# Kernel tuning notes

Measured on AMD Instinct MI355X. Metric: run time of the kernel, lower is better.

The kernel has to match this reference:

```python
import jax, jax.numpy as jnp
import numpy as np

B, N, DEG, E, Hd, IT = 512, 81, 20, 16, 96, 4


def sudoku_neighbors():
    # 20 constraint neighbors (row/col/box, excluding self) per cell of a 9x9 grid
    n = 9
    nbrs = []
    for r in range(n):
        for c in range(n):
            s = set()
            for k in range(n):
                s.add(r * n + k)
                s.add(k * n + c)
            br, bc = (r // 3) * 3, (c // 3) * 3
            for dr in range(3):
                for dc in range(3):
                    s.add((br + dr) * n + (bc + dc))
            s.discard(r * n + c)
            nbrs.append(sorted(s))
    return np.asarray(nbrs, dtype=np.int32)  # [81, 20]


def mlp3(x, w1, b1, w2, b2, w3, b3):
    # MLP([in, h, h, out]): ReLU between layers, linear output
    x = jax.nn.relu(x @ w1 + b1)
    x = jax.nn.relu(x @ w2 + b2)
    return x @ w3 + b3


def setup_inputs() -> dict:
    key = jax.random.key(0)
    ks = iter(jax.random.split(key, 64))
    W = lambda shape, s=0.05: jax.random.normal(next(ks), shape, jnp.float32) * s
    inp = {
        'grids': jax.random.randint(next(ks), (B, N), 0, 10),
        'nbr': jnp.asarray(sudoku_neighbors()),
        'iters': IT,
        'c0': jax.random.normal(next(ks), (B * N, Hd), jnp.float32),
        'embed_w': W((10, E), 1.0),
        'in_w1': W((E, Hd)), 'in_b1': jnp.zeros((Hd,)),
        'in_w2': W((Hd, Hd)), 'in_b2': jnp.zeros((Hd,)),
        'in_w3': W((Hd, Hd)), 'in_b3': jnp.zeros((Hd,)),
        'f_w1': W((2 * Hd, Hd)), 'f_b1': jnp.zeros((Hd,)),
        'f_w2': W((Hd, Hd)), 'f_b2': jnp.zeros((Hd,)),
        'f_w3': W((Hd, Hd)), 'f_b3': jnp.zeros((Hd,)),
        'g_w1': W((2 * Hd, Hd)), 'g_b1': jnp.zeros((Hd,)),
        'g_w2': W((Hd, Hd)), 'g_b2': jnp.zeros((Hd,)),
        'g_w3': W((Hd, Hd)), 'g_b3': jnp.zeros((Hd,)),
        'lstm_wih': W((Hd, 4 * Hd)), 'lstm_whh': W((Hd, 4 * Hd)),
        'lstm_bih': jnp.zeros((4 * Hd,)), 'lstm_bhh': jnp.zeros((4 * Hd,)),
        'r_w1': W((Hd, Hd)), 'r_b1': jnp.zeros((Hd,)),
        'r_w2': W((Hd, Hd)), 'r_b2': jnp.zeros((Hd,)),
        'r_w3': W((Hd, E)), 'r_b3': jnp.zeros((E,)),
    }
    return inp


def reference(grids, nbr, iters, c0, embed_w,
              in_w1, in_b1, in_w2, in_b2, in_w3, in_b3,
              f_w1, f_b1, f_w2, f_b2, f_w3, f_b3,
              g_w1, g_b1, g_w2, g_b2, g_w3, g_b3,
              lstm_wih, lstm_whh, lstm_bih, lstm_bhh,
              r_w1, r_b1, r_w2, r_b2, r_w3, r_b3):
    X = mlp3(embed_w[grids], in_w1, in_b1, in_w2, in_b2, in_w3, in_b3)  # [B,N,Hd]
    h0 = jax.lax.stop_gradient(X).reshape(B * N, Hd)  # H = X.clone().detach()
    c = c0  # [B*N, Hd]

    def step(carry, _):
        h, c = carry
        H = h.reshape(B, N, Hd)
        Hn = H[:, nbr]  # gather neighbor states [B,N,DEG,Hd]
        pair = jnp.concatenate(
            [jnp.broadcast_to(H[:, :, None, :], Hn.shape), Hn], axis=-1)  # [B,N,DEG,2Hd]
        M = mlp3(pair, f_w1, f_b1, f_w2, f_b2, f_w3, f_b3).sum(axis=2)  # [B,N,Hd]
        x_in = mlp3(jnp.concatenate([X, M], axis=-1),
                    g_w1, g_b1, g_w2, g_b2, g_w3, g_b3).reshape(B * N, Hd)
        gates = x_in @ lstm_wih + lstm_bih + h @ lstm_whh + lstm_bhh
        i, f, g, o = jnp.split(gates, 4, axis=-1)  # torch gate order i,f,g,o
        c2 = jax.nn.sigmoid(f) * c + jax.nn.sigmoid(i) * jnp.tanh(g)
        h2 = jax.nn.sigmoid(o) * jnp.tanh(c2)
        out = mlp3(h2.reshape(B, N, Hd), r_w1, r_b1, r_w2, r_b2, r_w3, r_b3)
        return (h2, c2), out

    _, outs = jax.lax.scan(step, (h0, c), None, length=iters)
    return outs  # [iters, B, N, E]
```

## Files before the change

kernel.cpp:

```cpp
#include <hip/hip_runtime.h>
#include <math.h>

#define Bsz 512
#define Nc  81
#define Rtot (Bsz*Nc)
#define DEG 20
#define Edim 16
#define HD  96
#define NITER 4

typedef __attribute__((ext_vector_type(8))) __bf16 bf16x8;
typedef __attribute__((ext_vector_type(4))) float f32x4;

__device__ __forceinline__ float sigf(float x){ return 1.0f/(1.0f+__expf(-x)); }
__device__ __forceinline__ float tanh_fast(float x){ return 2.0f/(1.0f+__expf(-2.0f*x)) - 1.0f; }

__device__ __forceinline__ unsigned short f2bf(float f){
    union{float f; unsigned u;} v; v.f=f;
    unsigned r = v.u + 0x7fff + ((v.u>>16)&1);
    return (unsigned short)(r>>16);
}
__device__ __forceinline__ float bf2f(unsigned short s){
    union{unsigned u; float f;} v; v.u=((unsigned)s)<<16; return v.f;
}
__device__ __forceinline__ bf16x8 pack8f(const float* x){
    bf16x8 r;
    #pragma unroll
    for (int j=0;j<8;j++) r[j]=(__bf16)x[j];
    return r;
}
__device__ __forceinline__ bf16x8 ldw(const __bf16* p){ return *(const bf16x8*)p; }

__device__ __forceinline__ int swz(int row, int col){
    return row*96 + ((((col>>2) ^ (row&7))<<2) | (col&3));
}
__device__ __forceinline__ void ldtr8(const float* tp, int row, int c, float* o){
    const int r96 = row*96, rho = row&7;
    const float4 a = *(const float4*)(tp + r96 + ((((c>>2)  ) ^ rho)<<2));
    const float4 b = *(const float4*)(tp + r96 + ((((c>>2)+1) ^ rho)<<2));
    o[0]=a.x;o[1]=a.y;o[2]=a.z;o[3]=a.w;o[4]=b.x;o[5]=b.y;o[6]=b.z;o[7]=b.w;
}
__device__ __forceinline__ bf16x8 packtr8(const float* tp, int row, int c){
    float t[8]; ldtr8(tp,row,c,t); return pack8f(t);
}

#define OFF_FW1T 0
#define OFF_FW2T 18432
#define OFF_FW3T 27648
#define OFF_GW1T 36864
#define OFF_GW2T 55296
#define OFF_GW3T 64512
#define OFF_WIHT 73728
#define OFF_WHHT 110592
#define OFF_RW1T 147456
#define OFF_RW2T 156672
#define OFF_RW3T 165888
#define WT_TOTAL 167424

__global__ __launch_bounds__(256) void k_prep(
    const float* __restrict__ fw1, const float* __restrict__ fw2, const float* __restrict__ fw3,
    const float* __restrict__ gw1, const float* __restrict__ gw2, const float* __restrict__ gw3,
    const float* __restrict__ wih, const float* __restrict__ whh,
    const float* __restrict__ rw1, const float* __restrict__ rw2, const float* __restrict__ rw3,
    __bf16* __restrict__ wt)
{
    int i = blockIdx.x*256 + threadIdx.x;
    if (i >= WT_TOTAL) return;
    int j = i;
    if (j < 18432){ int n=j/96, k=j-n*96;
        wt[OFF_FW1T+j] = (__bf16)(n<96 ? fw1[k*96+n] : fw1[(96+k)*96+(n-96)]); return; }
    j -= 18432;
    if (j < 9216){ int n=j/96, k=j-n*96; wt[OFF_FW2T+j]=(__bf16)fw2[k*96+n]; return; }
    j -= 9216;
    if (j < 9216){ int n=j/96, k=j-n*96; wt[OFF_FW3T+j]=(__bf16)fw3[k*96+n]; return; }
    j -= 9216;
    if (j < 18432){ int n=j/192, k=j-n*192; wt[OFF_GW1T+j]=(__bf16)gw1[k*96+n]; return; }
    j -= 18432;
    if (j < 9216){ int n=j/96, k=j-n*96; wt[OFF_GW2T+j]=(__bf16)gw2[k*96+n]; return; }
    j -= 9216;
    if (j < 9216){ int n=j/96, k=j-n*96; wt[OFF_GW3T+j]=(__bf16)gw3[k*96+n]; return; }
    j -= 9216;
    if (j < 36864){ int n=j/96, k=j-n*96; wt[OFF_WIHT+j]=(__bf16)wih[k*384+n]; return; }
    j -= 36864;
    if (j < 36864){ int n=j/96, k=j-n*96; wt[OFF_WHHT+j]=(__bf16)whh[k*384+n]; return; }
    j -= 36864;
    if (j < 9216){ int n=j/96, k=j-n*96; wt[OFF_RW1T+j]=(__bf16)rw1[k*96+n]; return; }
    j -= 9216;
    if (j < 9216){ int n=j/96, k=j-n*96; wt[OFF_RW2T+j]=(__bf16)rw2[k*96+n]; return; }
    j -= 9216;
    { int n=j/96, k=j-n*96; wt[OFF_RW3T+j]=(__bf16)rw3[k*16+n]; }
}

__global__ __launch_bounds__(192) void k_embed(
    const int* __restrict__ grids, const float* __restrict__ embw,
    const float* __restrict__ w1, const float* __restrict__ b1,
    const float* __restrict__ w2, const float* __restrict__ b2,
    const float* __restrict__ w3, const float* __restrict__ b3,
    const float* __restrict__ c0,
    __bf16* __restrict__ X, __bf16* __restrict__ H, float* __restrict__ C)
{
    __shared__ float e[2][4][Edim];
    __shared__ float a0[2][4][HD];
    __shared__ float a1[2][4][HD];
    const int tid = threadIdx.x;
    const int rg = tid / HD, c = tid - rg*HD;
    const int r0 = blockIdx.x*8 + rg*4;

    if (c < Edim) {
        #pragma unroll
        for (int rr=0;rr<4;rr++)
            e[rg][rr][c] = embw[grids[r0+rr]*Edim + c];
    }
    __syncthreads();
    float s0,s1,s2,s3;
    s0=s1=s2=s3=b1[c];
    #pragma unroll
    for (int k=0;k<Edim;k++){
        float w=w1[k*HD+c];
        s0+=e[rg][0][k]*w; s1+=e[rg][1][k]*w;
        s2+=e[rg][2][k]*w; s3+=e[rg][3][k]*w;
    }
    a0[rg][0][c]=fmaxf(s0,0.f); a0[rg][1][c]=fmaxf(s1,0.f);
    a0[rg][2][c]=fmaxf(s2,0.f); a0[rg][3][c]=fmaxf(s3,0.f);
    __syncthreads();
    s0=s1=s2=s3=b2[c];
    #pragma unroll 4
    for (int k=0;k<HD;k++){
        float w=w2[k*HD+c];
        s0+=a0[rg][0][k]*w; s1+=a0[rg][1][k]*w;
        s2+=a0[rg][2][k]*w; s3+=a0[rg][3][k]*w;
    }
    a1[rg][0][c]=fmaxf(s0,0.f); a1[rg][1][c]=fmaxf(s1,0.f);
    a1[rg][2][c]=fmaxf(s2,0.f); a1[rg][3][c]=fmaxf(s3,0.f);
    __syncthreads();
    s0=s1=s2=s3=b3[c];
    #pragma unroll 4
    for (int k=0;k<HD;k++){
        float w=w3[k*HD+c];
        s0+=a1[rg][0][k]*w; s1+=a1[rg][1][k]*w;
        s2+=a1[rg][2][k]*w; s3+=a1[rg][3][k]*w;
    }
    X[(r0+0)*HD+c]=(__bf16)s0; H[(r0+0)*HD+c]=(__bf16)s0; C[(r0+0)*HD+c]=c0[(r0+0)*HD+c];
    X[(r0+1)*HD+c]=(__bf16)s1; H[(r0+1)*HD+c]=(__bf16)s1; C[(r0+1)*HD+c]=c0[(r0+1)*HD+c];
    X[(r0+2)*HD+c]=(__bf16)s2; H[(r0+2)*HD+c]=(__bf16)s2; C[(r0+2)*HD+c]=c0[(r0+2)*HD+c];
    X[(r0+3)*HD+c]=(__bf16)s3; H[(r0+3)*HD+c]=(__bf16)s3; C[(r0+3)*HD+c]=c0[(r0+3)*HD+c];
}

__global__ __launch_bounds__(64) void k_ab(
    const __bf16* __restrict__ H, const __bf16* __restrict__ fw1t,
    __bf16* __restrict__ Ag, __bf16* __restrict__ Bmg)
{
    const int lane = threadIdx.x & 63;
    const int row16 = lane&15, kgrp = lane>>4, ko = kgrp*8;
    const int rowA = blockIdx.x*16 + row16;
    const int rowO = blockIdx.x*16 + kgrp*4;
    bf16x8 hf[3];
    #pragma unroll
    for (int kf=0;kf<3;kf++) hf[kf]=ldw(H + (size_t)rowA*HD + kf*32 + ko);
    #pragma unroll
    for (int nf=0;nf<12;nf++){
        f32x4 c={0.f,0.f,0.f,0.f};
        #pragma unroll
        for (int kf=0;kf<3;kf++)
            c=__builtin_amdgcn_mfma_f32_16x16x32_bf16(hf[kf], ldw(fw1t+(size_t)(nf*16+row16)*HD+kf*32+ko), c, 0,0,0);
        __bf16* dst = (nf<6)? Ag : Bmg;
        int col = ((nf<6)? nf : nf-6)*16 + row16;
        #pragma unroll
        for (int q=0;q<4;q++) dst[(size_t)(rowO+q)*HD+col]=(__bf16)c[q];
    }
}

__global__ __launch_bounds__(64) void k_edge(
    const __bf16* __restrict__ Ag, const __bf16* __restrict__ Bmg,
    const int* __restrict__ nbr,
    const float* __restrict__ fb1, const __bf16* __restrict__ fw2t,
    const float* __restrict__ fb2, const __bf16* __restrict__ fw3t,
    const float* __restrict__ fb3,
    __bf16* __restrict__ M)
{
    __shared__ float accs[16*96];
    const int lane = threadIdx.x & 63;
    const int row16 = lane&15, kgrp = lane>>4, ko = kgrp*8;
    const int rowA = blockIdx.x*16 + row16;
    const int iI = rowA % Nc;
    const __bf16* BmB = Bmg + (size_t)(rowA - iI)*HD;

    bf16x8 w2f[3][6];
    #pragma unroll
    for (int kf=0; kf<3; kf++)
        #pragma unroll
        for (int nf=0; nf<6; nf++)
            w2f[kf][nf] = ldw(fw2t + (size_t)(nf*16+row16)*HD + kf*32+ko);

    float a[3][8];
    #pragma unroll
    for (int kf=0;kf<3;kf++){
        bf16x8 av = ldw(Ag + (size_t)rowA*HD + kf*32 + ko);
        #pragma unroll
        for (int j=0;j<8;j++) a[kf][j] = (float)av[j] + fb1[kf*32+ko+j];
    }
    float b2c[6], b3c[6];
    #pragma unroll
    for (int nf=0;nf<6;nf++){ b2c[nf]=fb2[nf*16+row16]; b3c[nf]=20.0f*fb3[nf*16+row16]; }

    f32x4 acc[6];
    #pragma unroll
    for (int nf=0;nf<6;nf++) acc[nf]=(f32x4){0.f,0.f,0.f,0.f};

    const int* nrow = nbr + iI*DEG;
    #pragma unroll 2
    for (int d=0; d<DEG; d++){
        int j = nrow[d];
        const __bf16* Vb = BmB + (size_t)j*HD + ko;
        bf16x8 xf[3];
        #pragma unroll
        for (int kf=0;kf<3;kf++){
            bf16x8 v = ldw(Vb + kf*32);
            float t[8];
            #pragma unroll
            for (int jj=0;jj<8;jj++) t[jj]=fmaxf(a[kf][jj] + (float)v[jj], 0.f);
            xf[kf]=pack8f(t);
        }
        f32x4 c[6];
        #pragma unroll
        for (int nf=0;nf<6;nf++) c[nf]=(f32x4){0.f,0.f,0.f,0.f};
        #pragma unroll
        for (int kf=0;kf<3;kf++)
            #pragma unroll
            for (int nf=0;nf<6;nf++)
                c[nf]=__builtin_amdgcn_mfma_f32_16x16x32_bf16(xf[kf],w2f[kf][nf],c[nf],0,0,0);
        #pragma unroll
        for (int nf=0;nf<6;nf++)
            #pragma unroll
            for (int q2=0;q2<4;q2++)
                acc[nf][q2]+=fmaxf(c[nf][q2]+b2c[nf],0.f);
    }

    #pragma unroll
    for (int nf=0;nf<6;nf++)
        #pragma unroll
        for (int q2=0;q2<4;q2++)
            accs[swz(kgrp*4+q2, nf*16+row16)]=acc[nf][q2];
    __syncthreads();

    f32x4 c2[6];
    #pragma unroll
    for (int nf=0;nf<6;nf++) c2[nf]=(f32x4){0.f,0.f,0.f,0.f};
    #pragma unroll
    for (int kf=0;kf<3;kf++){
        float h[8]; ldtr8(accs, row16, kf*32+ko, h);
        bf16x8 hif, lof;
        #pragma unroll
        for (int j=0;j<8;j++){
            unsigned short hs=f2bf(h[j]);
            union{unsigned short s; __bf16 b;} u; u.s=hs;
            hif[j]=u.b; lof[j]=(__bf16)(h[j]-bf2f(hs));
        }
        #pragma unroll
        for (int nf=0;nf<6;nf++){
            bf16x8 w3f = ldw(fw3t + (size_t)(nf*16+row16)*HD + kf*32+ko);
            c2[nf]=__builtin_amdgcn_mfma_f32_16x16x32_bf16(hif,w3f,c2[nf],0,0,0);
            c2[nf]=__builtin_amdgcn_mfma_f32_16x16x32_bf16(lof,w3f,c2[nf],0,0,0);
        }
    }
    const int rowOut = blockIdx.x*16 + kgrp*4;
    #pragma unroll
    for (int nf=0;nf<6;nf++)
        #pragma unroll
        for (int q2=0;q2<4;q2++)
            M[(size_t)(rowOut+q2)*HD + nf*16+row16] = (__bf16)(c2[nf][q2]+b3c[nf]);
}

__global__ __launch_bounds__(64) void k_fused(
    const __bf16* __restrict__ Xg, const __bf16* __restrict__ Mg,
    __bf16* __restrict__ Hg, float* __restrict__ Cg,
    __bf16* __restrict__ Ag, __bf16* __restrict__ Bmg,
    const __bf16* __restrict__ wt,
    const float* __restrict__ gb1, const float* __restrict__ gb2, const float* __restrict__ gb3,
    const float* __restrict__ bih, const float* __restrict__ bhh,
    const float* __restrict__ rb1, const float* __restrict__ rb2, const float* __restrict__ rb3,
    float* __restrict__ out, int it)
{
    __shared__ float trs[2][16*96];
    const int lane = threadIdx.x & 63;
    const int row16 = lane&15, kgrp = lane>>4, ko = kgrp*8;
    const int r0 = blockIdx.x*32;
    const int rowA0 = r0+row16,   rowA1 = r0+16+row16;
    const int rowO0 = r0+kgrp*4,  rowO1 = r0+16+kgrp*4;
    float* tp0 = trs[0]; float* tp1 = trs[1];

    const __bf16* fw1t = wt + OFF_FW1T;
    const __bf16* gw1t = wt + OFF_GW1T;
    const __bf16* gw2t = wt + OFF_GW2T;
    const __bf16* gw3t = wt + OFF_GW3T;
    const __bf16* wiht = wt + OFF_WIHT;
    const __bf16* whht = wt + OFF_WHHT;
    const __bf16* rw1t = wt + OFF_RW1T;
    const __bf16* rw2t = wt + OFF_RW2T;
    const __bf16* rw3t = wt + OFF_RW3T;

    bf16x8 xa[6], xb[6];
    #pragma unroll
    for (int kf=0;kf<3;kf++){
        xa[kf]   = ldw(Xg + (size_t)rowA0*HD + kf*32+ko);
        xb[kf]   = ldw(Xg + (size_t)rowA1*HD + kf*32+ko);
        xa[3+kf] = ldw(Mg + (size_t)rowA0*HD + kf*32+ko);
        xb[3+kf] = ldw(Mg + (size_t)rowA1*HD + kf*32+ko);
    }
    #pragma unroll
    for (int nf=0;nf<6;nf++){
        f32x4 c0={0.f,0.f,0.f,0.f}, c1={0.f,0.f,0.f,0.f};
        #pragma unroll
        for (int kf=0;kf<6;kf++){
            bf16x8 wf = ldw(gw1t + (size_t)(nf*16+row16)*192 + kf*32+ko);
            c0=__builtin_amdgcn_mfma_f32_16x16x32_bf16(xa[kf],wf,c0,0,0,0);
            c1=__builtin_amdgcn_mfma_f32_16x16x32_bf16(xb[kf],wf,c1,0,0,0);
        }
        float b=gb1[nf*16+row16];
        #pragma unroll
        for (int q=0;q<4;q++){
            tp0[swz(kgrp*4+q, nf*16+row16)]=fmaxf(c0[q]+b,0.f);
            tp1[swz(kgrp*4+q, nf*16+row16)]=fmaxf(c1[q]+b,0.f);
        }
    }
    __syncthreads();
    bf16x8 ta[3], tb[3];
    #pragma unroll
    for (int kf=0;kf<3;kf++){ ta[kf]=packtr8(tp0,row16,kf*32+ko); tb[kf]=packtr8(tp1,row16,kf*32+ko); }
    __syncthreads();
    #pragma unroll
    for (int nf=0;nf<6;nf++){
        f32x4 c0={0.f,0.f,0.f,0.f}, c1={0.f,0.f,0.f,0.f};
        #pragma unroll
        for (int kf=0;kf<3;kf++){
            bf16x8 wf = ldw(gw2t + (size_t)(nf*16+row16)*HD + kf*32+ko);
            c0=__builtin_amdgcn_mfma_f32_16x16x32_bf16(ta[kf],wf,c0,0,0,0);
            c1=__builtin_amdgcn_mfma_f32_16x16x32_bf16(tb[kf],wf,c1,0,0,0);
        }
        float b=gb2[nf*16+row16];
        #pragma unroll
        for (int q=0;q<4;q++){
            tp0[swz(kgrp*4+q, nf*16+row16)]=fmaxf(c0[q]+b,0.f);
            tp1[swz(kgrp*4+q, nf*16+row16)]=fmaxf(c1[q]+b,0.f);
        }
    }
    __syncthreads();
    #pragma unroll
    for (int kf=0;kf<3;kf++){ ta[kf]=packtr8(tp0,row16,kf*32+ko); tb[kf]=packtr8(tp1,row16,kf*32+ko); }
    __syncthreads();
    #pragma unroll
    for (int nf=0;nf<6;nf++){
        f32x4 c0={0.f,0.f,0.f,0.f}, c1={0.f,0.f,0.f,0.f};
        #pragma unroll
        for (int kf=0;kf<3;kf++){
            bf16x8 wf = ldw(gw3t + (size_t)(nf*16+row16)*HD + kf*32+ko);
            c0=__builtin_amdgcn_mfma_f32_16x16x32_bf16(ta[kf],wf,c0,0,0,0);
            c1=__builtin_amdgcn_mfma_f32_16x16x32_bf16(tb[kf],wf,c1,0,0,0);
        }
        float b=gb3[nf*16+row16];
        #pragma unroll
        for (int q=0;q<4;q++){
            tp0[swz(kgrp*4+q, nf*16+row16)]=c0[q]+b;
            tp1[swz(kgrp*4+q, nf*16+row16)]=c1[q]+b;
        }
    }
    __syncthreads();
    bf16x8 xf0[3], xf1[3];
    #pragma unroll
    for (int kf=0;kf<3;kf++){ xf0[kf]=packtr8(tp0,row16,kf*32+ko); xf1[kf]=packtr8(tp1,row16,kf*32+ko); }
    __syncthreads();

    bf16x8 hfa[3], hfb[3];
    #pragma unroll
    for (int kf=0;kf<3;kf++){
        hfa[kf]=ldw(Hg + (size_t)rowA0*HD + kf*32+ko);
        hfb[kf]=ldw(Hg + (size_t)rowA1*HD + kf*32+ko);
    }
    #pragma unroll 2
    for (int nf=0;nf<6;nf++){
        const int col = nf*16+row16;
        f32x4 g0[4], g1[4];
        #pragma unroll
        for (int g=0;g<4;g++){ g0[g]=(f32x4){0.f,0.f,0.f,0.f}; g1[g]=(f32x4){0.f,0.f,0.f,0.f}; }
        #pragma unroll
        for (int g=0;g<4;g++){
            #pragma unroll
            for (int kf=0;kf<3;kf++){
                const int kk = kf*32+ko;
                bf16x8 wx = ldw(wiht + (size_t)(g*96+col)*HD + kk);
                bf16x8 wh = ldw(whht + (size_t)(g*96+col)*HD + kk);
                g0[g]=__builtin_amdgcn_mfma_f32_16x16x32_bf16(xf0[kf],wx,g0[g],0,0,0);
                g0[g]=__builtin_amdgcn_mfma_f32_16x16x32_bf16(hfa[kf],wh,g0[g],0,0,0);
                g1[g]=__builtin_amdgcn_mfma_f32_16x16x32_bf16(xf1[kf],wx,g1[g],0,0,0);
                g1[g]=__builtin_amdgcn_mfma_f32_16x16x32_bf16(hfb[kf],wh,g1[g],0,0,0);
            }
        }
        float bi=bih[    col]+bhh[    col];
        float bf=bih[ 96+col]+bhh[ 96+col];
        float bg=bih[192+col]+bhh[192+col];
        float bo=bih[288+col]+bhh[288+col];
        #pragma unroll
        for (int q=0;q<4;q++){
            {
                size_t idx=(size_t)(rowO0+q)*HD+col;
                float cold=Cg[idx];
                float iv=sigf(g0[0][q]+bi), fv=sigf(g0[1][q]+bf);
                float gv=tanh_fast(g0[2][q]+bg), ov=sigf(g0[3][q]+bo);
                float c2v=fv*cold+iv*gv;
                float h2v=ov*tanh_fast(c2v);
                Cg[idx]=c2v; Hg[idx]=(__bf16)h2v;
                tp0[swz(kgrp*4+q,col)]=h2v;
            }
            {
                size_t idx=(size_t)(rowO1+q)*HD+col;
                float cold=Cg[idx];
                float iv=sigf(g1[0][q]+bi), fv=sigf(g1[1][q]+bf);
                float gv=tanh_fast(g1[2][q]+bg), ov=sigf(g1[3][q]+bo);
                float c2v=fv*cold+iv*gv;
                float h2v=ov*tanh_fast(c2v);
                Cg[idx]=c2v; Hg[idx]=(__bf16)h2v;
                tp1[swz(kgrp*4+q,col)]=h2v;
            }
        }
    }
    __syncthreads();

    bf16x8 hf0[3], hf1[3];
    #pragma unroll
    for (int kf=0;kf<3;kf++){ hf0[kf]=packtr8(tp0,row16,kf*32+ko); hf1[kf]=packtr8(tp1,row16,kf*32+ko); }
    __syncthreads();

    if (it < NITER-1){
        #pragma unroll
        for (int nf=0;nf<12;nf++){
            f32x4 c0={0.f,0.f,0.f,0.f}, c1={0.f,0.f,0.f,0.f};
            #pragma unroll
            for (int kf=0;kf<3;kf++){
                bf16x8 wf = ldw(fw1t + (size_t)(nf*16+row16)*HD + kf*32+ko);
                c0=__builtin_amdgcn_mfma_f32_16x16x32_bf16(hf0[kf],wf,c0,0,0,0);
                c1=__builtin_amdgcn_mfma_f32_16x16x32_bf16(hf1[kf],wf,c1,0,0,0);
            }
            __bf16* dst = (nf<6)? Ag : Bmg;
            int col = ((nf<6)? nf : nf-6)*16 + row16;
            #pragma unroll
            for (int q=0;q<4;q++){
                dst[(size_t)(rowO0+q)*HD+col]=(__bf16)c0[q];
                dst[(size_t)(rowO1+q)*HD+col]=(__bf16)c1[q];
            }
        }
    }

    #pragma unroll
    for (int nf=0;nf<6;nf++){
        f32x4 c0={0.f,0.f,0.f,0.f}, c1={0.f,0.f,0.f,0.f};
        #pragma unroll
        for (int kf=0;kf<3;kf++){
            bf16x8 wf = ldw(rw1t + (size_t)(nf*16+row16)*HD + kf*32+ko);
            c0=__builtin_amdgcn_mfma_f32_16x16x32_bf16(hf0[kf],wf,c0,0,0,0);
            c1=__builtin_amdgcn_mfma_f32_16x16x32_bf16(hf1[kf],wf,c1,0,0,0);
        }
        float b=rb1[nf*16+row16];
        #pragma unroll
        for (int q=0;q<4;q++){
            tp0[swz(kgrp*4+q, nf*16+row16)]=fmaxf(c0[q]+b,0.f);
            tp1[swz(kgrp*4+q, nf*16+row16)]=fmaxf(c1[q]+b,0.f);
        }
    }
    __syncthreads();
    #pragma unroll
    for (int kf=0;kf<3;kf++){ ta[kf]=packtr8(tp0,row16,kf*32+ko); tb[kf]=packtr8(tp1,row16,kf*32+ko); }
    __syncthreads();
    #pragma unroll
    for (int nf=0;nf<6;nf++){
        f32x4 c0={0.f,0.f,0.f,0.f}, c1={0.f,0.f,0.f,0.f};
        #pragma unroll
        for (int kf=0;kf<3;kf++){
            bf16x8 wf = ldw(rw2t + (size_t)(nf*16+row16)*HD + kf*32+ko);
            c0=__builtin_amdgcn_mfma_f32_16x16x32_bf16(ta[kf],wf,c0,0,0,0);
            c1=__builtin_amdgcn_mfma_f32_16x16x32_bf16(tb[kf],wf,c1,0,0,0);
        }
        float b=rb2[nf*16+row16];
        #pragma unroll
        for (int q=0;q<4;q++){
            tp0[swz(kgrp*4+q, nf*16+row16)]=fmaxf(c0[q]+b,0.f);
            tp1[swz(kgrp*4+q, nf*16+row16)]=fmaxf(c1[q]+b,0.f);
        }
    }
    __syncthreads();
    #pragma unroll
    for (int kf=0;kf<3;kf++){ ta[kf]=packtr8(tp0,row16,kf*32+ko); tb[kf]=packtr8(tp1,row16,kf*32+ko); }
    {
        f32x4 c0={0.f,0.f,0.f,0.f}, c1={0.f,0.f,0.f,0.f};
        #pragma unroll
        for (int kf=0;kf<3;kf++){
            bf16x8 wf = ldw(rw3t + (size_t)row16*HD + kf*32+ko);
            c0=__builtin_amdgcn_mfma_f32_16x16x32_bf16(ta[kf],wf,c0,0,0,0);
            c1=__builtin_amdgcn_mfma_f32_16x16x32_bf16(tb[kf],wf,c1,0,0,0);
        }
        float b=rb3[row16];
        #pragma unroll
        for (int q=0;q<4;q++){
            out[((size_t)it*Rtot + rowO0+q)*Edim + row16]=c0[q]+b;
            out[((size_t)it*Rtot + rowO1+q)*Edim + row16]=c1[q]+b;
        }
    }
}

extern "C" void kernel_launch(void* const* d_in, const int* in_sizes, int n_in,
                              void* d_out, int out_size, void* d_ws, size_t ws_size,
                              hipStream_t stream) {
    const int*   grids  = (const int*)  d_in[0];
    const int*   nbr    = (const int*)  d_in[1];
    const float* c0     = (const float*)d_in[3];
    const float* embw   = (const float*)d_in[4];
    const float* in_w1  = (const float*)d_in[5];
    const float* in_b1  = (const float*)d_in[6];
    const float* in_w2  = (const float*)d_in[7];
    const float* in_b2  = (const float*)d_in[8];
    const float* in_w3  = (const float*)d_in[9];
    const float* in_b3  = (const float*)d_in[10];
    const float* f_w1   = (const float*)d_in[11];
    const float* f_b1   = (const float*)d_in[12];
    const float* f_w2   = (const float*)d_in[13];
    const float* f_b2   = (const float*)d_in[14];
    const float* f_w3   = (const float*)d_in[15];
    const float* f_b3   = (const float*)d_in[16];
    const float* g_b1   = (const float*)d_in[18];
    const float* g_w1   = (const float*)d_in[17];
    const float* g_w2   = (const float*)d_in[19];
    const float* g_b2   = (const float*)d_in[20];
    const float* g_w3   = (const float*)d_in[21];
    const float* g_b3   = (const float*)d_in[22];
    const float* wih    = (const float*)d_in[23];
    const float* whh    = (const float*)d_in[24];
    const float* bih    = (const float*)d_in[25];
    const float* bhh    = (const float*)d_in[26];
    const float* r_w1   = (const float*)d_in[27];
    const float* r_b1   = (const float*)d_in[28];
    const float* r_w2   = (const float*)d_in[29];
    const float* r_b2   = (const float*)d_in[30];
    const float* r_w3   = (const float*)d_in[31];
    const float* r_b3   = (const float*)d_in[32];

    __bf16* Xb = (__bf16*)d_ws;
    __bf16* Hb = Xb + (size_t)Rtot*HD;
    float*  Cw = (float*)(Hb + (size_t)Rtot*HD);
    __bf16* Aa = (__bf16*)(Cw + (size_t)Rtot*HD);
    __bf16* Bm = Aa + (size_t)Rtot*HD;
    __bf16* Mm = Bm + (size_t)Rtot*HD;
    __bf16* wt = Mm + (size_t)Rtot*HD;
    float* out = (float*)d_out;

    const __bf16* fw1t = wt + OFF_FW1T;
    const __bf16* fw2t = wt + OFF_FW2T;
    const __bf16* fw3t = wt + OFF_FW3T;

    hipLaunchKernelGGL(k_prep, dim3((WT_TOTAL+255)/256), dim3(256), 0, stream,
        f_w1, f_w2, f_w3, g_w1, g_w2, g_w3, wih, whh, r_w1, r_w2, r_w3, wt);

    hipLaunchKernelGGL(k_embed, dim3(Rtot/8), dim3(192), 0, stream,
        grids, embw, in_w1,in_b1,in_w2,in_b2,in_w3,in_b3, c0, Xb, Hb, Cw);

    hipLaunchKernelGGL(k_ab, dim3(Rtot/16), dim3(64), 0, stream,
        Hb, fw1t, Aa, Bm);

    for (int it=0; it<NITER; ++it){
        hipLaunchKernelGGL(k_edge, dim3(Rtot/16), dim3(64), 0, stream,
            Aa, Bm, nbr, f_b1, fw2t, f_b2, fw3t, f_b3, Mm);
        hipLaunchKernelGGL(k_fused, dim3(Rtot/32), dim3(64), 0, stream,
            Xb, Mm, Hb, Cw, Aa, Bm, wt,
            g_b1, g_b2, g_b3, bih, bhh, r_b1, r_b2, r_b3,
            out, it);
    }
}
```

Measured before the change: 485.6 us.

## Fuse embed MLP with first A/B projection via MFMA, prefetch edge neighbors, halve fused tile

The scalar fp32 embed MLP and the separate k_ab launch are replaced by one MFMA-based k_embed2 that computes X and the first f_w1 projections directly. The embedding is split into bf16 hi/lo parts to keep fp32-like precision in the first layer. The c0/H copies are removed by reading X and c0 directly on iteration 0. k_edge now software-prefetches the next neighbor's rows, and k_fused processes 16 rows per block instead of 32, doubling the grid at the cost of less weight reuse per block.

```diff
diff --git a/kernel.cpp b/kernel.cpp
--- a/kernel.cpp
+++ b/kernel.cpp
@@ -55,13 +55,17 @@
 #define OFF_RW1T 147456
 #define OFF_RW2T 156672
 #define OFF_RW3T 165888
-#define WT_TOTAL 167424
+#define OFF_IW1T 167424
+#define OFF_IW2T 170496
+#define OFF_IW3T 179712
+#define WT_TOTAL 188928
 
 __global__ __launch_bounds__(256) void k_prep(
     const float* __restrict__ fw1, const float* __restrict__ fw2, const float* __restrict__ fw3,
     const float* __restrict__ gw1, const float* __restrict__ gw2, const float* __restrict__ gw3,
     const float* __restrict__ wih, const float* __restrict__ whh,
     const float* __restrict__ rw1, const float* __restrict__ rw2, const float* __restrict__ rw3,
+    const float* __restrict__ iw1, const float* __restrict__ iw2, const float* __restrict__ iw3,
     __bf16* __restrict__ wt)
 {
     int i = blockIdx.x*256 + threadIdx.x;
@@ -88,81 +92,92 @@
     j -= 9216;
     if (j < 9216){ int n=j/96, k=j-n*96; wt[OFF_RW2T+j]=(__bf16)rw2[k*96+n]; return; }
     j -= 9216;
-    { int n=j/96, k=j-n*96; wt[OFF_RW3T+j]=(__bf16)rw3[k*16+n]; }
-}
-
-__global__ __launch_bounds__(192) void k_embed(
+    if (j < 1536){ int n=j/96, k=j-n*96; wt[OFF_RW3T+j]=(__bf16)rw3[k*16+n]; return; }
+    j -= 1536;
+    if (j < 3072){ int n=j>>5, k=j&31; wt[OFF_IW1T+j]=(__bf16)iw1[(k&15)*96+n]; return; }
+    j -= 3072;
+    if (j < 9216){ int n=j/96, k=j-n*96; wt[OFF_IW2T+j]=(__bf16)iw2[k*96+n]; return; }
+    j -= 9216;
+    { int n=j/96, k=j-n*96; wt[OFF_IW3T+j]=(__bf16)iw3[k*96+n]; }
+}
+
+__global__ __launch_bounds__(64) void k_embed2(
     const int* __restrict__ grids, const float* __restrict__ embw,
-    const float* __restrict__ w1, const float* __restrict__ b1,
-    const float* __restrict__ w2, const float* __restrict__ b2,
-    const float* __restrict__ w3, const float* __restrict__ b3,
-    const float* __restrict__ c0,
-    __bf16* __restrict__ X, __bf16* __restrict__ H, float* __restrict__ C)
+    const __bf16* __restrict__ wt,
+    const float* __restrict__ ib1, const float* __restrict__ ib2, const float* __restrict__ ib3,
+    __bf16* __restrict__ X, __bf16* __restrict__ Ag, __bf16* __restrict__ Bmg)
 {
-    __shared__ float e[2][4][Edim];
-    __shared__ float a0[2][4][HD];
-    __shared__ float a1[2][4][HD];
-    const int tid = threadIdx.x;
-    const int rg = tid / HD, c = tid - rg*HD;
-    const int r0 = blockIdx.x*8 + rg*4;
-
-    if (c < Edim) {
-        #pragma unroll
-        for (int rr=0;rr<4;rr++)
-            e[rg][rr][c] = embw[grids[r0+rr]*Edim + c];
-    }
-    __syncthreads();
-    float s0,s1,s2,s3;
-    s0=s1=s2=s3=b1[c];
-    #pragma unroll
-    for (int k=0;k<Edim;k++){
-        float w=w1[k*HD+c];
-        s0+=e[rg][0][k]*w; s1+=e[rg][1][k]*w;
-        s2+=e[rg][2][k]*w; s3+=e[rg][3][k]*w;
-    }
-    a0[rg][0][c]=fmaxf(s0,0.f); a0[rg][1][c]=fmaxf(s1,0.f);
-    a0[rg][2][c]=fmaxf(s2,0.f); a0[rg][3][c]=fmaxf(s3,0.f);
-    __syncthreads();
-    s0=s1=s2=s3=b2[c];
-    #pragma unroll 4
-    for (int k=0;k<HD;k++){
-        float w=w2[k*HD+c];
-        s0+=a0[rg][0][k]*w; s1+=a0[rg][1][k]*w;
-        s2+=a0[rg][2][k]*w; s3+=a0[rg][3][k]*w;
-    }
-    a1[rg][0][c]=fmaxf(s0,0.f); a1[rg][1][c]=fmaxf(s1,0.f);
-    a1[rg][2][c]=fmaxf(s2,0.f); a1[rg][3][c]=fmaxf(s3,0.f);
-    __syncthreads();
-    s0=s1=s2=s3=b3[c];
-    #pragma unroll 4
-    for (int k=0;k<HD;k++){
-        float w=w3[k*HD+c];
-        s0+=a1[rg][0][k]*w; s1+=a1[rg][1][k]*w;
-        s2+=a1[rg][2][k]*w; s3+=a1[rg][3][k]*w;
-    }
-    X[(r0+0)*HD+c]=(__bf16)s0; H[(r0+0)*HD+c]=(__bf16)s0; C[(r0+0)*HD+c]=c0[(r0+0)*HD+c];
-    X[(r0+1)*HD+c]=(__bf16)s1; H[(r0+1)*HD+c]=(__bf16)s1; C[(r0+1)*HD+c]=c0[(r0+1)*HD+c];
-    X[(r0+2)*HD+c]=(__bf16)s2; H[(r0+2)*HD+c]=(__bf16)s2; C[(r0+2)*HD+c]=c0[(r0+2)*HD+c];
-    X[(r0+3)*HD+c]=(__bf16)s3; H[(r0+3)*HD+c]=(__bf16)s3; C[(r0+3)*HD+c]=c0[(r0+3)*HD+c];
-}
-
-__global__ __launch_bounds__(64) void k_ab(
-    const __bf16* __restrict__ H, const __bf16* __restrict__ fw1t,
-    __bf16* __restrict__ Ag, __bf16* __restrict__ Bmg)
-{
+    __shared__ float tp[16*96];
     const int lane = threadIdx.x & 63;
     const int row16 = lane&15, kgrp = lane>>4, ko = kgrp*8;
     const int rowA = blockIdx.x*16 + row16;
     const int rowO = blockIdx.x*16 + kgrp*4;
+
+    const __bf16* iw1t = wt + OFF_IW1T;
+    const __bf16* iw2t = wt + OFF_IW2T;
+    const __bf16* iw3t = wt + OFF_IW3T;
+    const __bf16* fw1t = wt + OFF_FW1T;
+
+    const int g = grids[rowA];
+    const float* ew = embw + g*Edim + (kgrp&1)*8;
+    bf16x8 ef;
+    #pragma unroll
+    for (int j=0;j<8;j++){
+        float e = ew[j];
+        if (kgrp < 2) ef[j] = (__bf16)e;
+        else          ef[j] = (__bf16)(e - bf2f(f2bf(e)));
+    }
+    #pragma unroll
+    for (int nf=0;nf<6;nf++){
+        f32x4 c={0.f,0.f,0.f,0.f};
+        c=__builtin_amdgcn_mfma_f32_16x16x32_bf16(ef, ldw(iw1t+(size_t)(nf*16+row16)*32+ko), c,0,0,0);
+        float b=ib1[nf*16+row16];
+        #pragma unroll
+        for (int q=0;q<4;q++) tp[swz(kgrp*4+q, nf*16+row16)]=fmaxf(c[q]+b,0.f);
+    }
+    __syncthreads();
+    bf16x8 ta[3];
+    #pragma unroll
+    for (int kf=0;kf<3;kf++) ta[kf]=packtr8(tp,row16,kf*32+ko);
+    __syncthreads();
+    #pragma unroll
+    for (int nf=0;nf<6;nf++){
+        f32x4 c={0.f,0.f,0.f,0.f};
+        #pragma unroll
+        for (int kf=0;kf<3;kf++)
+            c=__builtin_amdgcn_mfma_f32_16x16x32_bf16(ta[kf], ldw(iw2t+(size_t)(nf*16+row16)*HD+kf*32+ko), c,0,0,0);
+        float b=ib2[nf*16+row16];
+        #pragma unroll
+        for (int q=0;q<4;q++) tp[swz(kgrp*4+q, nf*16+row16)]=fmaxf(c[q]+b,0.f);
+    }
+    __syncthreads();
+    #pragma unroll
+    for (int kf=0;kf<3;kf++) ta[kf]=packtr8(tp,row16,kf*32+ko);
+    __syncthreads();
+    #pragma unroll
+    for (int nf=0;nf<6;nf++){
+        f32x4 c={0.f,0.f,0.f,0.f};
+        #pragma unroll
+        for (int kf=0;kf<3;kf++)
+            c=__builtin_amdgcn_mfma_f32_16x16x32_bf16(ta[kf], ldw(iw3t+(size_t)(nf*16+row16)*HD+kf*32+ko), c,0,0,0);
+        float b=ib3[nf*16+row16];
+        #pragma unroll
+        for (int q=0;q<4;q++){
+            float v=c[q]+b;
+            X[(size_t)(rowO+q)*HD + nf*16+row16]=(__bf16)v;
+            tp[swz(kgrp*4+q, nf*16+row16)]=v;
+        }
+    }
+    __syncthreads();
     bf16x8 hf[3];
     #pragma unroll
-    for (int kf=0;kf<3;kf++) hf[kf]=ldw(H + (size_t)rowA*HD + kf*32 + ko);
+    for (int kf=0;kf<3;kf++) hf[kf]=packtr8(tp,row16,kf*32+ko);
     #pragma unroll
     for (int nf=0;nf<12;nf++){
         f32x4 c={0.f,0.f,0.f,0.f};
         #pragma unroll
         for (int kf=0;kf<3;kf++)
-            c=__builtin_amdgcn_mfma_f32_16x16x32_bf16(hf[kf], ldw(fw1t+(size_t)(nf*16+row16)*HD+kf*32+ko), c, 0,0,0);
+            c=__builtin_amdgcn_mfma_f32_16x16x32_bf16(hf[kf], ldw(fw1t+(size_t)(nf*16+row16)*HD+kf*32+ko), c,0,0,0);
         __bf16* dst = (nf<6)? Ag : Bmg;
         int col = ((nf<6)? nf : nf-6)*16 + row16;
         #pragma unroll
@@ -183,7 +198,7 @@
     const int row16 = lane&15, kgrp = lane>>4, ko = kgrp*8;
     const int rowA = blockIdx.x*16 + row16;
     const int iI = rowA % Nc;
-    const __bf16* BmB = Bmg + (size_t)(rowA - iI)*HD;
+    const __bf16* BmB = Bmg + (size_t)(rowA - iI)*HD + ko;
 
     bf16x8 w2f[3][6];
     #pragma unroll
@@ -208,18 +223,31 @@
     for (int nf=0;nf<6;nf++) acc[nf]=(f32x4){0.f,0.f,0.f,0.f};
 
     const int* nrow = nbr + iI*DEG;
+    bf16x8 v0,v1,v2;
+    {
+        const __bf16* Vb = BmB + (size_t)nrow[0]*HD;
+        v0=ldw(Vb); v1=ldw(Vb+32); v2=ldw(Vb+64);
+    }
     #pragma unroll 2
     for (int d=0; d<DEG; d++){
-        int j = nrow[d];
-        const __bf16* Vb = BmB + (size_t)j*HD + ko;
+        bf16x8 n0,n1,n2;
+        {
+            int dn = (d+1<DEG)? d+1 : 0;
+            const __bf16* Vb = BmB + (size_t)nrow[dn]*HD;
+            n0=ldw(Vb); n1=ldw(Vb+32); n2=ldw(Vb+64);
+        }
         bf16x8 xf[3];
-        #pragma unroll
-        for (int kf=0;kf<3;kf++){
-            bf16x8 v = ldw(Vb + kf*32);
+        {
             float t[8];
             #pragma unroll
-            for (int jj=0;jj<8;jj++) t[jj]=fmaxf(a[kf][jj] + (float)v[jj], 0.f);
-            xf[kf]=pack8f(t);
+            for (int jj=0;jj<8;jj++) t[jj]=fmaxf(a[0][jj]+(float)v0[jj],0.f);
+            xf[0]=pack8f(t);
+            #pragma unroll
+            for (int jj=0;jj<8;jj++) t[jj]=fmaxf(a[1][jj]+(float)v1[jj],0.f);
+            xf[1]=pack8f(t);
+            #pragma unroll
+            for (int jj=0;jj<8;jj++) t[jj]=fmaxf(a[2][jj]+(float)v2[jj],0.f);
+            xf[2]=pack8f(t);
         }
         f32x4 c[6];
         #pragma unroll
@@ -234,6 +262,7 @@
             #pragma unroll
             for (int q2=0;q2<4;q2++)
                 acc[nf][q2]+=fmaxf(c[nf][q2]+b2c[nf],0.f);
+        v0=n0; v1=n1; v2=n2;
     }
 
     #pragma unroll
@@ -273,21 +302,20 @@
 
 __global__ __launch_bounds__(64) void k_fused(
     const __bf16* __restrict__ Xg, const __bf16* __restrict__ Mg,
-    __bf16* __restrict__ Hg, float* __restrict__ Cg,
+    const __bf16* __restrict__ Hin, __bf16* __restrict__ Hout,
+    const float* __restrict__ Cin, float* __restrict__ Cout,
     __bf16* __restrict__ Ag, __bf16* __restrict__ Bmg,
     const __bf16* __restrict__ wt,
     const float* __restrict__ gb1, const float* __restrict__ gb2, const float* __restrict__ gb3,
     const float* __restrict__ bih, const float* __restrict__ bhh,
     const float* __restrict__ rb1, const float* __restrict__ rb2, const float* __restrict__ rb3,
-    float* __restrict__ out, int it)
+    float* __restrict__ out, int it, int wab)
 {
-    __shared__ float trs[2][16*96];
+    __shared__ float tp[16*96];
     const int lane = threadIdx.x & 63;
     const int row16 = lane&15, kgrp = lane>>4, ko = kgrp*8;
-    const int r0 = blockIdx.x*32;
-    const int rowA0 = r0+row16,   rowA1 = r0+16+row16;
-    const int rowO0 = r0+kgrp*4,  rowO1 = r0+16+kgrp*4;
-    float* tp0 = trs[0]; float* tp1 = trs[1];
+    const int rowA = blockIdx.x*16 + row16;
+    const int rowO = blockIdx.x*16 + kgrp*4;
 
     const __bf16* fw1t = wt + OFF_FW1T;
     const __bf16* gw1t = wt + OFF_GW1T;
@@ -299,100 +327,74 @@
     const __bf16* rw2t = wt + OFF_RW2T;
     const __bf16* rw3t = wt + OFF_RW3T;
 
-    bf16x8 xa[6], xb[6];
+    bf16x8 xm[6];
     #pragma unroll
     for (int kf=0;kf<3;kf++){
-        xa[kf]   = ldw(Xg + (size_t)rowA0*HD + kf*32+ko);
-        xb[kf]   = ldw(Xg + (size_t)rowA1*HD + kf*32+ko);
-        xa[3+kf] = ldw(Mg + (size_t)rowA0*HD + kf*32+ko);
-        xb[3+kf] = ldw(Mg + (size_t)rowA1*HD + kf*32+ko);
-    }
-    #pragma unroll
-    for (int nf=0;nf<6;nf++){
-        f32x4 c0={0.f,0.f,0.f,0.f}, c1={0.f,0.f,0.f,0.f};
-        #pragma unroll
-        for (int kf=0;kf<6;kf++){
-            bf16x8 wf = ldw(gw1t + (size_t)(nf*16+row16)*192 + kf*32+ko);
-            c0=__builtin_amdgcn_mfma_f32_16x16x32_bf16(xa[kf],wf,c0,0,0,0);
-            c1=__builtin_amdgcn_mfma_f32_16x16x32_bf16(xb[kf],wf,c1,0,0,0);
-        }
+        xm[kf]   = ldw(Xg + (size_t)rowA*HD + kf*32+ko);
+        xm[3+kf] = ldw(Mg + (size_t)rowA*HD + kf*32+ko);
+    }
+    #pragma unroll
+    for (int nf=0;nf<6;nf++){
+        f32x4 c={0.f,0.f,0.f,0.f};
+        #pragma unroll
+        for (int kf=0;kf<6;kf++)
+            c=__builtin_amdgcn_mfma_f32_16x16x32_bf16(xm[kf], ldw(gw1t+(size_t)(nf*16+row16)*192+kf*32+ko), c,0,0,0);
         float b=gb1[nf*16+row16];
         #pragma unroll
-        for (int q=0;q<4;q++){
-            tp0[swz(kgrp*4+q, nf*16+row16)]=fmaxf(c0[q]+b,0.f);
-            tp1[swz(kgrp*4+q, nf*16+row16)]=fmaxf(c1[q]+b,0.f);
-        }
-    }
-    __syncthreads();
-    bf16x8 ta[3], tb[3];
-    #pragma unroll
-    for (int kf=0;kf<3;kf++){ ta[kf]=packtr8(tp0,row16,kf*32+ko); tb[kf]=packtr8(tp1,row16,kf*32+ko); }
-    __syncthreads();
-    #pragma unroll
-    for (int nf=0;nf<6;nf++){
-        f32x4 c0={0.f,0.f,0.f,0.f}, c1={0.f,0.f,0.f,0.f};
-        #pragma unroll
-        for (int kf=0;kf<3;kf++){
-            bf16x8 wf = ldw(gw2t + (size_t)(nf*16+row16)*HD + kf*32+ko);
-            c0=__builtin_amdgcn_mfma_f32_16x16x32_bf16(ta[kf],wf,c0,0,0,0);
-            c1=__builtin_amdgcn_mfma_f32_16x16x32_bf16(tb[kf],wf,c1,0,0,0);
-        }
+        for (int q=0;q<4;q++) tp[swz(kgrp*4+q, nf*16+row16)]=fmaxf(c[q]+b,0.f);
+    }
+    __syncthreads();
+    bf16x8 ta[3];
+    #pragma unroll
+    for (int kf=0;kf<3;kf++) ta[kf]=packtr8(tp,row16,kf*32+ko);
+    __syncthreads();
+    #pragma unroll
+    for (int nf=0;nf<6;nf++){
+        f32x4 c={0.f,0.f,0.f,0.f};
+        #pragma unroll
+        for (int kf=0;kf<3;kf++)
+            c=__builtin_amdgcn_mfma_f32_16x16x32_bf16(ta[kf], ldw(gw2t+(size_t)(nf*16+row16)*HD+kf*32+ko), c,0,0,0);
         float b=gb2[nf*16+row16];
         #pragma unroll
-        for (int q=0;q<4;q++){
-            tp0[swz(kgrp*4+q, nf*16+row16)]=fmaxf(c0[q]+b,0.f);
-            tp1[swz(kgrp*4+q, nf*16+row16)]=fmaxf(c1[q]+b,0.f);
-        }
-    }
-    __syncthreads();
-    #pragma unroll
-    for (int kf=0;kf<3;kf++){ ta[kf]=packtr8(tp0,row16,kf*32+ko); tb[kf]=packtr8(tp1,row16,kf*32+ko); }
-    __syncthreads();
-    #pragma unroll
-    for (int nf=0;nf<6;nf++){
-        f32x4 c0={0.f,0.f,0.f,0.f}, c1={0.f,0.f,0.f,0.f};
-        #pragma unroll
-        for (int kf=0;kf<3;kf++){
-            bf16x8 wf = ldw(gw3t + (size_t)(nf*16+row16)*HD + kf*32+ko);
-            c0=__builtin_amdgcn_mfma_f32_16x16x32_bf16(ta[kf],wf,c0,0,0,0);
-            c1=__builtin_amdgcn_mfma_f32_16x16x32_bf16(tb[kf],wf,c1,0,0,0);
-        }
+        for (int q=0;q<4;q++) tp[swz(kgrp*4+q, nf*16+row16)]=fmaxf(c[q]+b,0.f);
+    }
+    __syncthreads();
+    #pragma unroll
+    for (int kf=0;kf<3;kf++) ta[kf]=packtr8(tp,row16,kf*32+ko);
+    __syncthreads();
+    #pragma unroll
+    for (int nf=0;nf<6;nf++){
+        f32x4 c={0.f,0.f,0.f,0.f};
+        #pragma unroll
+        for (int kf=0;kf<3;kf++)
+            c=__builtin_amdgcn_mfma_f32_16x16x32_bf16(ta[kf], ldw(gw3t+(size_t)(nf*16+row16)*HD+kf*32+ko), c,0,0,0);
         float b=gb3[nf*16+row16];
         #pragma unroll
-        for (int q=0;q<4;q++){
-            tp0[swz(kgrp*4+q, nf*16+row16)]=c0[q]+b;
-            tp1[swz(kgrp*4+q, nf*16+row16)]=c1[q]+b;
-        }
-    }
-    __syncthreads();
-    bf16x8 xf0[3], xf1[3];
-    #pragma unroll
-    for (int kf=0;kf<3;kf++){ xf0[kf]=packtr8(tp0,row16,kf*32+ko); xf1[kf]=packtr8(tp1,row16,kf*32+ko); }
-    __syncthreads();
-
-    bf16x8 hfa[3], hfb[3];
-    #pragma unroll
-    for (int kf=0;kf<3;kf++){
-        hfa[kf]=ldw(Hg + (size_t)rowA0*HD + kf*32+ko);
-        hfb[kf]=ldw(Hg + (size_t)rowA1*HD + kf*32+ko);
-    }
+        for (int q=0;q<4;q++) tp[swz(kgrp*4+q, nf*16+row16)]=c[q]+b;
+    }
+    __syncthreads();
+    bf16x8 xf[3];
+    #pragma unroll
+    for (int kf=0;kf<3;kf++) xf[kf]=packtr8(tp,row16,kf*32+ko);
+    __syncthreads();
+
+    bf16x8 hfa[3];
+    #pragma unroll
+    for (int kf=0;kf<3;kf++) hfa[kf]=ldw(Hin + (size_t)rowA*HD + kf*32+ko);
+
     #pragma unroll 2
     for (int nf=0;nf<6;nf++){
         const int col = nf*16+row16;
-        f32x4 g0[4], g1[4];
-        #pragma unroll
-        for (int g=0;g<4;g++){ g0[g]=(f32x4){0.f,0.f,0.f,0.f}; g1[g]=(f32x4){0.f,0.f,0.f,0.f}; }
+        f32x4 g4[4];
+        #pragma unroll
+        for (int g=0;g<4;g++) g4[g]=(f32x4){0.f,0.f,0.f,0.f};
         #pragma unroll
         for (int g=0;g<4;g++){
             #pragma unroll
             for (int kf=0;kf<3;kf++){
                 const int kk = kf*32+ko;
-                bf16x8 wx = ldw(wiht + (size_t)(g*96+col)*HD + kk);
-                bf16x8 wh = ldw(whht + (size_t)(g*96+col)*HD + kk);
-                g0[g]=__builtin_amdgcn_mfma_f32_16x16x32_bf16(xf0[kf],wx,g0[g],0,0,0);
-                g0[g]=__builtin_amdgcn_mfma_f32_16x16x32_bf16(hfa[kf],wh,g0[g],0,0,0);
-                g1[g]=__builtin_amdgcn_mfma_f32_16x16x32_bf16(xf1[kf],wx,g1[g],0,0,0);
-                g1[g]=__builtin_amdgcn_mfma_f32_16x16x32_bf16(hfb[kf],wh,g1[g],0,0,0);
+                g4[g]=__builtin_amdgcn_mfma_f32_16x16x32_bf16(xf[kf],  ldw(wiht+(size_t)(g*96+col)*HD+kk), g4[g],0,0,0);
+                g4[g]=__builtin_amdgcn_mfma_f32_16x16x32_bf16(hfa[kf], ldw(whht+(size_t)(g*96+col)*HD+kk), g4[g],0,0,0);
             }
         }
         float bi=bih[    col]+bhh[    col];
@@ -401,108 +403,73 @@
         float bo=bih[288+col]+bhh[288+col];
         #pragma unroll
         for (int q=0;q<4;q++){
-            {
-                size_t idx=(size_t)(rowO0+q)*HD+col;
-                float cold=Cg[idx];
-                float iv=sigf(g0[0][q]+bi), fv=sigf(g0[1][q]+bf);
-                float gv=tanh_fast(g0[2][q]+bg), ov=sigf(g0[3][q]+bo);
-                float c2v=fv*cold+iv*gv;
-                float h2v=ov*tanh_fast(c2v);
-                Cg[idx]=c2v; Hg[idx]=(__bf16)h2v;
-                tp0[swz(kgrp*4+q,col)]=h2v;
-            }
-            {
-                size_t idx=(size_t)(rowO1+q)*HD+col;
-                float cold=Cg[idx];
-                float iv=sigf(g1[0][q]+bi), fv=sigf(g1[1][q]+bf);
-                float gv=tanh_fast(g1[2][q]+bg), ov=sigf(g1[3][q]+bo);
-                float c2v=fv*cold+iv*gv;
-                float h2v=ov*tanh_fast(c2v);
-                Cg[idx]=c2v; Hg[idx]=(__bf16)h2v;
-                tp1[swz(kgrp*4+q,col)]=h2v;
-            }
-        }
-    }
-    __syncthreads();
-
-    bf16x8 hf0[3], hf1[3];
-    #pragma unroll
-    for (int kf=0;kf<3;kf++){ hf0[kf]=packtr8(tp0,row16,kf*32+ko); hf1[kf]=packtr8(tp1,row16,kf*32+ko); }
-    __syncthreads();
-
-    if (it < NITER-1){
+            size_t idx=(size_t)(rowO+q)*HD+col;
+            float cold=Cin[idx];
+            float iv=sigf(g4[0][q]+bi), fv=sigf(g4[1][q]+bf);
+            float gv=tanh_fast(g4[2][q]+bg), ov=sigf(g4[3][q]+bo);
+            float c2v=fv*cold+iv*gv;
+            float h2v=ov*tanh_fast(c2v);
+            Cout[idx]=c2v; Hout[idx]=(__bf16)h2v;
+            tp[swz(kgrp*4+q,col)]=h2v;
+        }
+    }
+    __syncthreads();
+
+    bf16x8 hf[3];
+    #pragma unroll
+    for (int kf=0;kf<3;kf++) hf[kf]=packtr8(tp,row16,kf*32+ko);
+    __syncthreads();
+
+    if (wab){
         #pragma unroll
         for (int nf=0;nf<12;nf++){
-            f32x4 c0={0.f,0.f,0.f,0.f}, c1={0.f,0.f,0.f,0.f};
-            #pragma unroll
-            for (int kf=0;kf<3;kf++){
-                bf16x8 wf = ldw(fw1t + (size_t)(nf*16+row16)*HD + kf*32+ko);
-                c0=__builtin_amdgcn_mfma_f32_16x16x32_bf16(hf0[kf],wf,c0,0,0,0);
-                c1=__builtin_amdgcn_mfma_f32_16x16x32_bf16(hf1[kf],wf,c1,0,0,0);
-            }
+            f32x4 c={0.f,0.f,0.f,0.f};
+            #pragma unroll
+            for (int kf=0;kf<3;kf++)
+                c=__builtin_amdgcn_mfma_f32_16x16x32_bf16(hf[kf], ldw(fw1t+(size_t)(nf*16+row16)*HD+kf*32+ko), c,0,0,0);
             __bf16* dst = (nf<6)? Ag : Bmg;
             int col = ((nf<6)? nf : nf-6)*16 + row16;
             #pragma unroll
-            for (int q=0;q<4;q++){
-                dst[(size_t)(rowO0+q)*HD+col]=(__bf16)c0[q];
-                dst[(size_t)(rowO1+q)*HD+col]=(__bf16)c1[q];
-            }
-        }
-    }
-
-    #pragma unroll
-    for (int nf=0;nf<6;nf++){
-        f32x4 c0={0.f,0.f,0.f,0.f}, c1={0.f,0.f,0.f,0.f};
-        #pragma unroll
-        for (int kf=0;kf<3;kf++){
-            bf16x8 wf = ldw(rw1t + (size_t)(nf*16+row16)*HD + kf*32+ko);
-            c0=__builtin_amdgcn_mfma_f32_16x16x32_bf16(hf0[kf],wf,c0,0,0,0);
-            c1=__builtin_amdgcn_mfma_f32_16x16x32_bf16(hf1[kf],wf,c1,0,0,0);
-        }
+            for (int q=0;q<4;q++) dst[(size_t)(rowO+q)*HD+col]=(__bf16)c[q];
+        }
+    }
+
+    #pragma unroll
+    for (int nf=0;nf<6;nf++){
+        f32x4 c={0.f,0.f,0.f,0.f};
+        #pragma unroll
+        for (int kf=0;kf<3;kf++)
+            c=__builtin_amdgcn_mfma_f32_16x16x32_bf16(hf[kf], ldw(rw1t+(size_t)(nf*16+row16)*HD+kf*32+ko), c,0,0,0);
         float b=rb1[nf*16+row16];
         #pragma unroll
-        for (int q=0;q<4;q++){
-            tp0[swz(kgrp*4+q, nf*16+row16)]=fmaxf(c0[q]+b,0.f);
-            tp1[swz(kgrp*4+q, nf*16+row16)]=fmaxf(c1[q]+b,0.f);
-        }
-    }
-    __syncthreads();
-    #pragma unroll
-    for (int kf=0;kf<3;kf++){ ta[kf]=packtr8(tp0,row16,kf*32+ko); tb[kf]=packtr8(tp1,row16,kf*32+ko); }
-    __syncthreads();
-    #pragma unroll
-    for (int nf=0;nf<6;nf++){
-        f32x4 c0={0.f,0.f,0.f,0.f}, c1={0.f,0.f,0.f,0.f};
-        #pragma unroll
-        for (int kf=0;kf<3;kf++){
-            bf16x8 wf = ldw(rw2t + (size_t)(nf*16+row16)*HD + kf*32+ko);
-            c0=__builtin_amdgcn_mfma_f32_16x16x32_bf16(ta[kf],wf,c0,0,0,0);
-            c1=__builtin_amdgcn_mfma_f32_16x16x32_bf16(tb[kf],wf,c1,0,0,0);
-        }
+        for (int q=0;q<4;q++) tp[swz(kgrp*4+q, nf*16+row16)]=fmaxf(c[q]+b,0.f);
+    }
+    __syncthreads();
+    #pragma unroll
+    for (int kf=0;kf<3;kf++) ta[kf]=packtr8(tp,row16,kf*32+ko);
+    __syncthreads();
+    #pragma unroll
+    for (int nf=0;nf<6;nf++){
+        f32x4 c={0.f,0.f,0.f,0.f};
+        #pragma unroll
+        for (int kf=0;kf<3;kf++)
+            c=__builtin_amdgcn_mfma_f32_16x16x32_bf16(ta[kf], ldw(rw2t+(size_t)(nf*16+row16)*HD+kf*32+ko), c,0,0,0);
         float b=rb2[nf*16+row16];
         #pragma unroll
-        for (int q=0;q<4;q++){
-            tp0[swz(kgrp*4+q, nf*16+row16)]=fmaxf(c0[q]+b,0.f);
-            tp1[swz(kgrp*4+q, nf*16+row16)]=fmaxf(c1[q]+b,0.f);
-        }
-    }
-    __syncthreads();
-    #pragma unroll
-    for (int kf=0;kf<3;kf++){ ta[kf]=packtr8(tp0,row16,kf*32+ko); tb[kf]=packtr8(tp1,row16,kf*32+ko); }
+        for (int q=0;q<4;q++) tp[swz(kgrp*4+q, nf*16+row16)]=fmaxf(c[q]+b,0.f);
+    }
+    __syncthreads();
+    #pragma unroll
+    for (int kf=0;kf<3;kf++) ta[kf]=packtr8(tp,row16,kf*32+ko);
     {
-        f32x4 c0={0.f,0.f,0.f,0.f}, c1={0.f,0.f,0.f,0.f};
-        #pragma unroll
-        for (int kf=0;kf<3;kf++){
-            bf16x8 wf = ldw(rw3t + (size_t)row16*HD + kf*32+ko);
-            c0=__builtin_amdgcn_mfma_f32_16x16x32_bf16(ta[kf],wf,c0,0,0,0);
-            c1=__builtin_amdgcn_mfma_f32_16x16x32_bf16(tb[kf],wf,c1,0,0,0);
-        }
+        f32x4 c={0.f,0.f,0.f,0.f};
+        #pragma unroll
+        for (int kf=0;kf<3;kf++)
+            c=__builtin_amdgcn_mfma_f32_16x16x32_bf16(ta[kf], ldw(rw3t+(size_t)row16*HD+kf*32+ko), c,0,0,0);
         float b=rb3[row16];
         #pragma unroll
-        for (int q=0;q<4;q++){
-            out[((size_t)it*Rtot + rowO0+q)*Edim + row16]=c0[q]+b;
-            out[((size_t)it*Rtot + rowO1+q)*Edim + row16]=c1[q]+b;
-        }
+        for (int q=0;q<4;q++)
+            out[((size_t)it*Rtot + rowO+q)*Edim + row16]=c[q]+b;
     }
 }
 
@@ -525,8 +492,8 @@
     const float* f_b2   = (const float*)d_in[14];
     const float* f_w3   = (const float*)d_in[15];
     const float* f_b3   = (const float*)d_in[16];
+    const float* g_w1   = (const float*)d_in[17];
     const float* g_b1   = (const float*)d_in[18];
-    const float* g_w1   = (const float*)d_in[17];
     const float* g_w2   = (const float*)d_in[19];
     const float* g_b2   = (const float*)d_in[20];
     const float* g_w3   = (const float*)d_in[21];
@@ -551,25 +518,25 @@
     __bf16* wt = Mm + (size_t)Rtot*HD;
     float* out = (float*)d_out;
 
-    const __bf16* fw1t = wt + OFF_FW1T;
     const __bf16* fw2t = wt + OFF_FW2T;
     const __bf16* fw3t = wt + OFF_FW3T;
 
     hipLaunchKernelGGL(k_prep, dim3((WT_TOTAL+255)/256), dim3(256), 0, stream,
-        f_w1, f_w2, f_w3, g_w1, g_w2, g_w3, wih, whh, r_w1, r_w2, r_w3, wt);
-
-    hipLaunchKernelGGL(k_embed, dim3(Rtot/8), dim3(192), 0, stream,
-        grids, embw, in_w1,in_b1,in_w2,in_b2,in_w3,in_b3, c0, Xb, Hb, Cw);
-
-    hipLaunchKernelGGL(k_ab, dim3(Rtot/16), dim3(64), 0, stream,
-        Hb, fw1t, Aa, Bm);
+        f_w1, f_w2, f_w3, g_w1, g_w2, g_w3, wih, whh, r_w1, r_w2, r_w3,
+        in_w1, in_w2, in_w3, wt);
+
+    hipLaunchKernelGGL(k_embed2, dim3(Rtot/16), dim3(64), 0, stream,
+        grids, embw, wt, in_b1, in_b2, in_b3, Xb, Aa, Bm);
 
     for (int it=0; it<NITER; ++it){
         hipLaunchKernelGGL(k_edge, dim3(Rtot/16), dim3(64), 0, stream,
             Aa, Bm, nbr, f_b1, fw2t, f_b2, fw3t, f_b3, Mm);
-        hipLaunchKernelGGL(k_fused, dim3(Rtot/32), dim3(64), 0, stream,
-            Xb, Mm, Hb, Cw, Aa, Bm, wt,
+        hipLaunchKernelGGL(k_fused, dim3(Rtot/16), dim3(64), 0, stream,
+            Xb, Mm,
+            (it==0)? Xb : Hb, Hb,
+            (it==0)? c0 : Cw, Cw,
+            Aa, Bm, wt,
             g_b1, g_b2, g_b3, bih, bhh, r_b1, r_b2, r_b3,
-            out, it);
-    }
-}
+            out, it, (it<NITER-1)?1:0);
+    }
+}
```

New measurement: 506.0 us. 1.04x slower.
